# Kernel optimization log

Hardware: AMD Instinct MI355X
Metric: run time of the kernel (lower is better)

## Reference

```python
import jax, jax.numpy as jnp
import numpy as np

N_EMBED = 1024
EMBED_DIM = 64
BETA = 0.25


def setup_inputs() -> dict:
    key = jax.random.key(0)
    k1, k2 = jax.random.split(key)
    x = jax.random.normal(k1, (32, EMBED_DIM, 64, 64), dtype=jnp.float32)  # NCHW, C == embed_dim
    embed = jax.random.uniform(
        k2, (N_EMBED, EMBED_DIM), dtype=jnp.float32,
        minval=-1.0 / N_EMBED, maxval=1.0 / N_EMBED,
    )
    return {"x": x, "embed": embed}


def reference(x, embed):
    # NCHW -> NHWC, flatten spatial+batch to rows of embed_dim
    z = jnp.transpose(x, (0, 2, 3, 1))                      # [B,H,W,D]
    zf = z.reshape(-1, EMBED_DIM)                           # [N,D]
    # squared L2 distance to every codeword: ||z||^2 + ||e||^2 - 2 z.e
    dist = (
        jnp.sum(zf * zf, axis=1, keepdims=True)
        + jnp.sum(embed * embed, axis=1)
        - 2.0 * zf @ embed.T
    )                                                       # [N, n_embed]
    idx = jnp.argmin(dist, axis=1)                          # [N]
    # one-hot @ embed == direct gather (same math, no scatter/matmul)
    z_q = embed[idx].reshape(z.shape)                       # [B,H,W,D]
    sg = jax.lax.stop_gradient
    loss = jnp.mean((sg(z_q) - z) ** 2) + BETA * jnp.mean((z_q - sg(z)) ** 2)
    # straight-through estimator
    z_q = z + sg(z_q - z)
    z_q = jnp.transpose(z_q, (0, 3, 1, 2))                  # back to NCHW
    return (z_q, loss)
```

## Files before the change

kernel.cpp:

```cpp
#include <hip/hip_runtime.h>


#define TOTAL_ELEMS 8388608
#define LOSS_SCALE (1.25f / 8388608.f)

typedef float  f32x4  __attribute__((ext_vector_type(4)));
typedef unsigned int u32x2 __attribute__((ext_vector_type(2)));

static __device__ __forceinline__ void gload_lds16(const void* g, void* l) {
    __builtin_amdgcn_global_load_lds(
        (const __attribute__((address_space(1))) void*)g,
        (__attribute__((address_space(3))) void*)l,
        16, 0, 0);
}

__global__ void vq_prep(const float* __restrict__ embed,
                        unsigned char* __restrict__ eb,
                        float* __restrict__ c0,
                        float* __restrict__ loss_slot) {
    int t   = blockIdx.x * 256 + threadIdx.x;
    int row = t >> 2, qd = t & 3;
    const float* src = embed + row * 64 + qd * 16;
    float s = 0.f;
    unsigned int d[4];
#pragma unroll
    for (int i = 0; i < 4; i++) {
        f32x4 v = *(const f32x4*)(src + i * 4);
        s += v[0]*v[0] + v[1]*v[1] + v[2]*v[2] + v[3]*v[3];
        unsigned int r = 0;
        r = __builtin_amdgcn_cvt_pk_fp8_f32(v[0] * 1024.f, v[1] * 1024.f, r, false);
        r = __builtin_amdgcn_cvt_pk_fp8_f32(v[2] * 1024.f, v[3] * 1024.f, r, true);
        d[i] = r;
    }
    char* dstb = (char*)eb + row * 64;
    const int sw = (row & 7) << 3;
    u32x2 lo = {d[0], d[1]}, hi = {d[2], d[3]};
    *(u32x2*)(dstb + ((qd * 16) ^ sw))     = lo;
    *(u32x2*)(dstb + ((qd * 16 + 8) ^ sw)) = hi;
    s += __shfl_xor(s, 1);
    s += __shfl_xor(s, 2);
    if (qd == 0) c0[row] = 64.f - 512.f * s;
    if (t == 0) *loss_slot = 0.f;
}

__global__ __launch_bounds__(512, 4) void vq_main(
    const float* __restrict__ x,
    const float* __restrict__ embed,
    const unsigned char* __restrict__ eb,
    const float* __restrict__ c0,
    float* __restrict__ out,
    float* __restrict__ loss) {

    __shared__ __align__(16) unsigned char cb[65536];
    __shared__ __align__(16) float c0l[1024];
    __shared__ float lpart[8];

    const int t    = threadIdx.x;
    const int wv   = t >> 6, lane = t & 63;
    const int l15  = lane & 15, lq = lane >> 4;

    const int blk = blockIdx.x;
    const int b   = blk >> 4;
    const int h0  = (blk & 15) * 4;
    const size_t xbase = (size_t)b * 262144 + (size_t)h0 * 64;
    const size_t rowoff = (size_t)(wv >> 1) * 64 + (wv & 1) * 32;

    const char* ebp = (const char*)eb;

#pragma unroll
    for (int s = 0; s < 8; s++)
        gload_lds16(ebp + s * 8192 + t * 16, &cb[s * 8192 + t * 16]);

    if (t < 256) *(f32x4*)(c0l + t * 4) = *(const f32x4*)(c0 + t * 4);

    float part = 0.f;
    unsigned long long bfr[2][2];
#pragma unroll
    for (int nt = 0; nt < 2; nt++) {
#pragma unroll
        for (int kh = 0; kh < 2; kh++) {
            unsigned int dw[2];
#pragma unroll
            for (int p = 0; p < 2; p++) {
                float f[4];
#pragma unroll
                for (int j = 0; j < 4; j++) {
                    f[j] = x[xbase + (size_t)(kh * 32 + lq * 8 + p * 4 + j) * 4096
                             + rowoff + nt * 16 + l15];
                    part += f[j] * f[j];
                }
                unsigned int r = 0;
                r = __builtin_amdgcn_cvt_pk_fp8_f32(f[0], f[1], r, false);
                r = __builtin_amdgcn_cvt_pk_fp8_f32(f[2], f[3], r, true);
                dw[p] = r;
            }
            bfr[nt][kh] = (unsigned long long)dw[0] | ((unsigned long long)dw[1] << 32);
        }
    }
    __syncthreads();

    unsigned int key[2] = {0u, 0u};
    const int swz = (l15 & 7) << 3;
#pragma unroll 8
    for (int mt = 0; mt < 64; mt++) {
        const unsigned char* rp = &cb[(mt * 16 + l15) * 64];
        long a0 = *(const long*)(rp + ((lq * 8) ^ swz));
        long a1 = *(const long*)(rp + ((32 + lq * 8) ^ swz));
        f32x4 c0v = *(const f32x4*)(c0l + mt * 16 + lq * 4);
        const int invm = 1023 - mt * 16 - lq * 4;
#pragma unroll
        for (int nt = 0; nt < 2; nt++) {
            f32x4 acc = __builtin_amdgcn_mfma_f32_16x16x32_fp8_fp8(
                a0, (long)bfr[nt][0], c0v, 0, 0, 0);
            acc = __builtin_amdgcn_mfma_f32_16x16x32_fp8_fp8(
                a1, (long)bfr[nt][1], acc, 0, 0, 0);
#pragma unroll
            for (int r = 0; r < 4; r++) {
                unsigned int k2 = (__float_as_uint(acc[r]) & 0xFFFFFC00u)
                                | (unsigned int)(invm - r);
                key[nt] = key[nt] > k2 ? key[nt] : k2;
            }
        }
    }

#pragma unroll
    for (int nt = 0; nt < 2; nt++) {
        unsigned int k = key[nt];
        unsigned int o = (unsigned int)__shfl_xor((int)k, 16); k = k > o ? k : o;
        o = (unsigned int)__shfl_xor((int)k, 32);              k = k > o ? k : o;
        key[nt] = k;
        part -= (1.f / 2048.f) * __uint_as_float(k & 0xFFFFFC00u);
    }

    unsigned int ks = ((lane >> 4) & 1) ? key[1] : key[0];
    const int idx = 1023 - (int)(ks & 1023u);

#pragma unroll
    for (int off = 1; off < 64; off <<= 1) part += __shfl_xor(part, off);
    if (lane == 0) lpart[wv] = part;

    const int ch0 = (lane >> 5) * 32;
    const float* erow = embed + idx * 64 + ch0;
    float* orow = out + xbase + rowoff + (lane & 31) + (size_t)ch0 * 4096;
#pragma unroll
    for (int c4 = 0; c4 < 8; c4++) {
        f32x4 ev = *(const f32x4*)(erow + c4 * 4);
#pragma unroll
        for (int j = 0; j < 4; j++)
            orow[(size_t)(c4 * 4 + j) * 4096] = ev[j];
    }

    __syncthreads();
    if (t == 0) {
        float s = 0.f;
#pragma unroll
        for (int i = 0; i < 8; i++) s += lpart[i];
        atomicAdd(loss, (s + 32.0f) * LOSS_SCALE);
    }
}

extern "C" void kernel_launch(void* const* d_in, const int* in_sizes, int n_in,
                              void* d_out, int out_size, void* d_ws, size_t ws_size,
                              hipStream_t stream) {
    const float* x     = (const float*)d_in[0];
    const float* embed = (const float*)d_in[1];
    unsigned char* eb  = (unsigned char*)d_ws;
    float* c0          = (float*)((char*)d_ws + 65536);
    float* out  = (float*)d_out;
    float* loss = out + TOTAL_ELEMS;

    vq_prep<<<16, 256, 0, stream>>>(embed, eb, c0, loss);
    vq_main<<<512, 512, 0, stream>>>(x, embed, eb, c0, out, loss);
}
```

Measured before the change: 34.75 us.

## Halve block to 4 waves, each handling 64 rows, with 16-byte codebook LDS reads

```diff
diff --git a/kernel.cpp b/kernel.cpp
--- a/kernel.cpp
+++ b/kernel.cpp
@@ -5,7 +5,8 @@
 #define LOSS_SCALE (1.25f / 8388608.f)
 
 typedef float  f32x4  __attribute__((ext_vector_type(4)));
-typedef unsigned int u32x2 __attribute__((ext_vector_type(2)));
+typedef unsigned int u32x4 __attribute__((ext_vector_type(4)));
+typedef long   longx2 __attribute__((ext_vector_type(2)));
 
 static __device__ __forceinline__ void gload_lds16(const void* g, void* l) {
     __builtin_amdgcn_global_load_lds(
@@ -14,36 +15,42 @@
         16, 0, 0);
 }
 
+static __device__ __forceinline__ unsigned int umax(unsigned int a, unsigned int b) {
+    return a > b ? a : b;
+}
+
 __global__ void vq_prep(const float* __restrict__ embed,
                         unsigned char* __restrict__ eb,
                         float* __restrict__ c0,
                         float* __restrict__ loss_slot) {
     int t   = blockIdx.x * 256 + threadIdx.x;
     int row = t >> 2, qd = t & 3;
-    const float* src = embed + row * 64 + qd * 16;
-    float s = 0.f;
-    unsigned int d[4];
-#pragma unroll
-    for (int i = 0; i < 4; i++) {
-        f32x4 v = *(const f32x4*)(src + i * 4);
-        s += v[0]*v[0] + v[1]*v[1] + v[2]*v[2] + v[3]*v[3];
-        unsigned int r = 0;
-        r = __builtin_amdgcn_cvt_pk_fp8_f32(v[0] * 1024.f, v[1] * 1024.f, r, false);
-        r = __builtin_amdgcn_cvt_pk_fp8_f32(v[2] * 1024.f, v[3] * 1024.f, r, true);
-        d[i] = r;
-    }
-    char* dstb = (char*)eb + row * 64;
-    const int sw = (row & 7) << 3;
-    u32x2 lo = {d[0], d[1]}, hi = {d[2], d[3]};
-    *(u32x2*)(dstb + ((qd * 16) ^ sw))     = lo;
-    *(u32x2*)(dstb + ((qd * 16 + 8) ^ sw)) = hi;
+    const float* s0 = embed + row * 64 + qd * 8;
+    const float* s1 = embed + row * 64 + 32 + qd * 8;
+    f32x4 v0 = *(const f32x4*)s0, v1 = *(const f32x4*)(s0 + 4);
+    f32x4 w0 = *(const f32x4*)s1, w1 = *(const f32x4*)(s1 + 4);
+    float s = v0[0]*v0[0] + v0[1]*v0[1] + v0[2]*v0[2] + v0[3]*v0[3]
+            + v1[0]*v1[0] + v1[1]*v1[1] + v1[2]*v1[2] + v1[3]*v1[3]
+            + w0[0]*w0[0] + w0[1]*w0[1] + w0[2]*w0[2] + w0[3]*w0[3]
+            + w1[0]*w1[0] + w1[1]*w1[1] + w1[2]*w1[2] + w1[3]*w1[3];
+    unsigned int d0 = 0, d1 = 0, d2 = 0, d3 = 0;
+    d0 = __builtin_amdgcn_cvt_pk_fp8_f32(v0[0]*1024.f, v0[1]*1024.f, d0, false);
+    d0 = __builtin_amdgcn_cvt_pk_fp8_f32(v0[2]*1024.f, v0[3]*1024.f, d0, true);
+    d1 = __builtin_amdgcn_cvt_pk_fp8_f32(v1[0]*1024.f, v1[1]*1024.f, d1, false);
+    d1 = __builtin_amdgcn_cvt_pk_fp8_f32(v1[2]*1024.f, v1[3]*1024.f, d1, true);
+    d2 = __builtin_amdgcn_cvt_pk_fp8_f32(w0[0]*1024.f, w0[1]*1024.f, d2, false);
+    d2 = __builtin_amdgcn_cvt_pk_fp8_f32(w0[2]*1024.f, w0[3]*1024.f, d2, true);
+    d3 = __builtin_amdgcn_cvt_pk_fp8_f32(w1[0]*1024.f, w1[1]*1024.f, d3, false);
+    d3 = __builtin_amdgcn_cvt_pk_fp8_f32(w1[2]*1024.f, w1[3]*1024.f, d3, true);
+    u32x4 o = {d0, d1, d2, d3};
+    *(u32x4*)((char*)eb + row * 64 + qd * 16) = o;
     s += __shfl_xor(s, 1);
     s += __shfl_xor(s, 2);
     if (qd == 0) c0[row] = 64.f - 512.f * s;
     if (t == 0) *loss_slot = 0.f;
 }
 
-__global__ __launch_bounds__(512, 4) void vq_main(
+__global__ __launch_bounds__(256, 2) void vq_main(
     const float* __restrict__ x,
     const float* __restrict__ embed,
     const unsigned char* __restrict__ eb,
@@ -53,7 +60,7 @@
 
     __shared__ __align__(16) unsigned char cb[65536];
     __shared__ __align__(16) float c0l[1024];
-    __shared__ float lpart[8];
+    __shared__ float lpart[4];
 
     const int t    = threadIdx.x;
     const int wv   = t >> 6, lane = t & 63;
@@ -63,20 +70,19 @@
     const int b   = blk >> 4;
     const int h0  = (blk & 15) * 4;
     const size_t xbase = (size_t)b * 262144 + (size_t)h0 * 64;
-    const size_t rowoff = (size_t)(wv >> 1) * 64 + (wv & 1) * 32;
 
     const char* ebp = (const char*)eb;
 
 #pragma unroll
-    for (int s = 0; s < 8; s++)
-        gload_lds16(ebp + s * 8192 + t * 16, &cb[s * 8192 + t * 16]);
+    for (int s = 0; s < 16; s++)
+        gload_lds16(ebp + s * 4096 + t * 16, &cb[s * 4096 + t * 16]);
 
-    if (t < 256) *(f32x4*)(c0l + t * 4) = *(const f32x4*)(c0 + t * 4);
+    *(f32x4*)(c0l + t * 4) = *(const f32x4*)(c0 + t * 4);
 
     float part = 0.f;
-    unsigned long long bfr[2][2];
+    long bfr[4][2];
 #pragma unroll
-    for (int nt = 0; nt < 2; nt++) {
+    for (int nt = 0; nt < 4; nt++) {
 #pragma unroll
         for (int kh = 0; kh < 2; kh++) {
             unsigned int dw[2];
@@ -86,7 +92,7 @@
 #pragma unroll
                 for (int j = 0; j < 4; j++) {
                     f[j] = x[xbase + (size_t)(kh * 32 + lq * 8 + p * 4 + j) * 4096
-                             + rowoff + nt * 16 + l15];
+                             + (size_t)wv * 64 + nt * 16 + l15];
                     part += f[j] * f[j];
                 }
                 unsigned int r = 0;
@@ -94,56 +100,55 @@
                 r = __builtin_amdgcn_cvt_pk_fp8_f32(f[2], f[3], r, true);
                 dw[p] = r;
             }
-            bfr[nt][kh] = (unsigned long long)dw[0] | ((unsigned long long)dw[1] << 32);
+            bfr[nt][kh] = (long)(((unsigned long long)dw[1] << 32) | dw[0]);
         }
     }
     __syncthreads();
 
-    unsigned int key[2] = {0u, 0u};
-    const int swz = (l15 & 7) << 3;
+    unsigned int key[4] = {0u, 0u, 0u, 0u};
+    const unsigned char* abase = &cb[l15 * 64 + lq * 16];
+    const float* cbase = c0l + lq * 4;
 #pragma unroll 8
     for (int mt = 0; mt < 64; mt++) {
-        const unsigned char* rp = &cb[(mt * 16 + l15) * 64];
-        long a0 = *(const long*)(rp + ((lq * 8) ^ swz));
-        long a1 = *(const long*)(rp + ((32 + lq * 8) ^ swz));
-        f32x4 c0v = *(const f32x4*)(c0l + mt * 16 + lq * 4);
+        longx2 av = *(const longx2*)(abase + mt * 1024);
+        f32x4 c0v = *(const f32x4*)(cbase + mt * 16);
         const int invm = 1023 - mt * 16 - lq * 4;
 #pragma unroll
-        for (int nt = 0; nt < 2; nt++) {
+        for (int nt = 0; nt < 4; nt++) {
             f32x4 acc = __builtin_amdgcn_mfma_f32_16x16x32_fp8_fp8(
-                a0, (long)bfr[nt][0], c0v, 0, 0, 0);
+                av[0], bfr[nt][0], c0v, 0, 0, 0);
             acc = __builtin_amdgcn_mfma_f32_16x16x32_fp8_fp8(
-                a1, (long)bfr[nt][1], acc, 0, 0, 0);
-#pragma unroll
-            for (int r = 0; r < 4; r++) {
-                unsigned int k2 = (__float_as_uint(acc[r]) & 0xFFFFFC00u)
-                                | (unsigned int)(invm - r);
-                key[nt] = key[nt] > k2 ? key[nt] : k2;
-            }
+                av[1], bfr[nt][1], acc, 0, 0, 0);
+            unsigned int k0 = (__float_as_uint(acc[0]) & 0xFFFFFC00u) | (unsigned int)(invm);
+            unsigned int k1 = (__float_as_uint(acc[1]) & 0xFFFFFC00u) | (unsigned int)(invm - 1);
+            unsigned int k2 = (__float_as_uint(acc[2]) & 0xFFFFFC00u) | (unsigned int)(invm - 2);
+            unsigned int k3 = (__float_as_uint(acc[3]) & 0xFFFFFC00u) | (unsigned int)(invm - 3);
+            key[nt] = umax(key[nt], umax(umax(k0, k1), umax(k2, k3)));
         }
     }
 
 #pragma unroll
-    for (int nt = 0; nt < 2; nt++) {
+    for (int nt = 0; nt < 4; nt++) {
         unsigned int k = key[nt];
-        unsigned int o = (unsigned int)__shfl_xor((int)k, 16); k = k > o ? k : o;
-        o = (unsigned int)__shfl_xor((int)k, 32);              k = k > o ? k : o;
+        unsigned int o = (unsigned int)__shfl_xor((int)k, 16); k = umax(k, o);
+        o = (unsigned int)__shfl_xor((int)k, 32);              k = umax(k, o);
         key[nt] = k;
         part -= (1.f / 2048.f) * __uint_as_float(k & 0xFFFFFC00u);
     }
 
-    unsigned int ks = ((lane >> 4) & 1) ? key[1] : key[0];
+    unsigned int klo = (lane & 16) ? key[1] : key[0];
+    unsigned int khi = (lane & 16) ? key[3] : key[2];
+    unsigned int ks  = (lane & 32) ? khi : klo;
     const int idx = 1023 - (int)(ks & 1023u);
 
 #pragma unroll
     for (int off = 1; off < 64; off <<= 1) part += __shfl_xor(part, off);
     if (lane == 0) lpart[wv] = part;
 
-    const int ch0 = (lane >> 5) * 32;
-    const float* erow = embed + idx * 64 + ch0;
-    float* orow = out + xbase + rowoff + (lane & 31) + (size_t)ch0 * 4096;
+    const float* erow = embed + idx * 64;
+    float* orow = out + xbase + (size_t)wv * 64 + lane;
 #pragma unroll
-    for (int c4 = 0; c4 < 8; c4++) {
+    for (int c4 = 0; c4 < 16; c4++) {
         f32x4 ev = *(const f32x4*)(erow + c4 * 4);
 #pragma unroll
         for (int j = 0; j < 4; j++)
@@ -152,10 +157,7 @@
 
     __syncthreads();
     if (t == 0) {
-        float s = 0.f;
-#pragma unroll
-        for (int i = 0; i < 8; i++) s += lpart[i];
-        atomicAdd(loss, (s + 32.0f) * LOSS_SCALE);
+        atomicAdd(loss, (lpart[0] + lpart[1] + lpart[2] + lpart[3] + 32.0f) * LOSS_SCALE);
     }
 }
 
@@ -170,5 +172,5 @@
     float* loss = out + TOTAL_ELEMS;
 
     vq_prep<<<16, 256, 0, stream>>>(embed, eb, c0, loss);
-    vq_main<<<512, 512, 0, stream>>>(x, embed, eb, c0, out, loss);
+    vq_main<<<512, 256, 0, stream>>>(x, embed, eb, c0, out, loss);
 }
```

After: 37.06 us. 6.6% more time.
